# Kernel tuning notes

Hardware: AMD Instinct MI355X
Metric: run time of the kernel (lower is better)

Reference implementation:

```python
import jax, jax.numpy as jnp
import numpy as np

B, T, SEQ = 8, 129, 128
H, N, NL, NE, V = 512, 64, 4, 128, 18

def _gelu(x):
    return jax.nn.gelu(x, approximate=False)

def _conv2d(x, w, b, stride):
    y = jax.lax.conv_general_dilated(x, w, (stride, stride), 'VALID',
                                     dimension_numbers=('NCHW', 'OIHW', 'NCHW'))
    return y + b[None, :, None, None]

def _layernorm(x, g, b, eps=1e-5):
    mu = jnp.mean(x, axis=-1, keepdims=True)
    var = jnp.mean(jnp.square(x - mu), axis=-1, keepdims=True)
    return (x - mu) * jax.lax.rsqrt(var + eps) * g + b

def _s4_kernel(log_dt, A_re, A_im, C_re, C_im, L):
    # Diagonal SSM (ZOH discretization, B=1): K[h,l] = 2*Re(sum_n Ceff * exp(dt*A)^l)
    dt = jnp.exp(log_dt)[:, None]                  # [H,1]
    A = A_re + 1j * A_im                            # [H,N] complex64
    dtA = (dt * A).astype(jnp.complex64)
    C = (C_re + 1j * C_im).astype(jnp.complex64)
    Ceff = C * (jnp.exp(dtA) - 1.0) / A             # [H,N]
    vand = jnp.exp(dtA[:, :, None] * jnp.arange(L, dtype=jnp.float32))  # [H,N,L]
    return 2.0 * jnp.einsum('hn,hnl->hl', Ceff, vand).real

def _fft_conv(u, K, D):
    # u: [B,H,L]  K: [H,L]  causal conv via zero-padded FFT
    L = u.shape[-1]
    n = 2 * L
    Uf = jnp.fft.rfft(u, n=n)
    Kf = jnp.fft.rfft(K, n=n)
    y = jnp.fft.irfft(Uf * Kf[None], n=n)[..., :L]
    return y + D[None, :, None] * u

def setup_inputs() -> dict:
    key = jax.random.key(0)
    ks = jax.random.split(key, 32)
    d = {}
    d['states'] = jax.random.uniform(ks[0], (B, T, 4, 84, 84), dtype=jnp.float32)
    d['actions'] = jax.random.randint(ks[1], (B, T), 0, V)
    d['rtgs'] = jax.random.uniform(ks[2], (B, T, 1), dtype=jnp.float32)
    s = 0.02
    d['enc_w1'] = jax.random.normal(ks[3], (32, 4, 8, 8)) * s
    d['enc_b1'] = jnp.zeros((32,))
    d['enc_w2'] = jax.random.normal(ks[4], (64, 32, 4, 4)) * s
    d['enc_b2'] = jnp.zeros((64,))
    d['enc_w3'] = jax.random.normal(ks[5], (64, 64, 3, 3)) * s
    d['enc_b3'] = jnp.zeros((64,))
    d['enc_lw'] = jax.random.normal(ks[6], (3136, NE)) * s
    d['enc_lb'] = jnp.zeros((NE,))
    d['ret_w'] = jax.random.normal(ks[7], (1, NE)) * s
    d['ret_b'] = jnp.zeros((NE,))
    d['act_emb'] = jax.random.normal(ks[8], (V, NE)) * s
    d['proj_w'] = jax.random.normal(ks[9], (3 * NE, H)) * s
    d['proj_b'] = jnp.zeros((H,))
    d['pre_w'] = jax.random.normal(ks[10], (H, H)) * s
    d['pre_b'] = jnp.zeros((H,))
    d['ln_g'] = jnp.ones((NL, H))
    d['ln_b'] = jnp.zeros((NL, H))
    lo, hi = np.log(1e-3), np.log(1e-1)
    d['log_dt'] = lo + jax.random.uniform(ks[11], (NL, H)) * (hi - lo)
    d['A_re'] = -0.5 * jnp.ones((NL, H, N))
    d['A_im'] = jnp.broadcast_to(np.pi * jnp.arange(N, dtype=jnp.float32), (NL, H, N)).copy()
    d['C_re'] = jax.random.normal(ks[12], (NL, H, N)) * (0.5 ** 0.5)
    d['C_im'] = jax.random.normal(ks[13], (NL, H, N)) * (0.5 ** 0.5)
    d['Dp'] = jax.random.normal(ks[14], (NL, H))
    d['aft_w'] = jax.random.normal(ks[15], (NL, H, H)) * s
    d['aft_b'] = jnp.zeros((NL, H))
    d['out_w'] = jax.random.normal(ks[16], (H, V)) * s
    return d

def reference(states, actions, rtgs, enc_w1, enc_b1, enc_w2, enc_b2, enc_w3, enc_b3,
              enc_lw, enc_lb, ret_w, ret_b, act_emb, proj_w, proj_b, pre_w, pre_b,
              ln_g, ln_b, log_dt, A_re, A_im, C_re, C_im, Dp, aft_w, aft_b, out_w):
    S = actions.shape[1] - 1  # del_r = 1
    # state encoder over B*S frames
    x = states[:, 1:].reshape(-1, 4, 84, 84)
    x = jax.nn.relu(_conv2d(x, enc_w1, enc_b1, 4))
    x = jax.nn.relu(_conv2d(x, enc_w2, enc_b2, 2))
    x = jax.nn.relu(_conv2d(x, enc_w3, enc_b3, 1))
    se = jnp.tanh(x.reshape(x.shape[0], -1) @ enc_lw + enc_lb)          # [B*S, NE]
    ae = jnp.tanh(act_emb[actions[:, :S].reshape(-1)])                   # [B*S, NE]
    re = jnp.tanh(rtgs[:, :S].reshape(-1, 1) @ ret_w + ret_b)            # [B*S, NE]
    u = jnp.concatenate([se, ae, re], axis=-1) @ proj_w + proj_b
    u = u.reshape(states.shape[0], S, H)
    y = _gelu(u) @ pre_w + pre_b                                          # beforeblock
    for i in range(NL):
        r = _layernorm(y, ln_g[i], ln_b[i])
        v = jnp.transpose(r, (0, 2, 1))                                   # [B,H,S]
        K = _s4_kernel(log_dt[i], A_re[i], A_im[i], C_re[i], C_im[i], S)
        c = _fft_conv(v, K, Dp[i])
        c = jnp.transpose(c, (0, 2, 1))                                   # [B,S,H]
        c = _gelu(_gelu(c) @ aft_w[i] + aft_b[i])
        y = c + y                                                          # s4_resnet
    logits = y @ out_w                                                     # [B,S,V]
    return logits
```

## Files before the change

kernel.cpp:

```cpp
#include <hip/hip_runtime.h>

#define Bq 8
#define Tq 129
#define Sq 128
#define Hq 512
#define Nq 64
#define NLq 4
#define NEq 128
#define Vq 18

typedef unsigned short u16;
typedef unsigned int u32;
typedef __attribute__((ext_vector_type(8))) short short8v;
typedef __attribute__((ext_vector_type(4))) float f32x4;

__device__ __forceinline__ float gelu_f(float x) {
  return 0.5f * x * (1.0f + erff(x * 0.70710678118654752f));
}

__device__ __forceinline__ u16 f2b(float x) {
  union { float f; unsigned int u; } v; v.f = x;
  unsigned int r = v.u + 0x7FFFu + ((v.u >> 16) & 1u);
  return (u16)(r >> 16);
}

__device__ __forceinline__ float b2f_lo(u32 u) {
  union { unsigned int u; float f; } v; v.u = u << 16; return v.f;
}
__device__ __forceinline__ float b2f_hi(u32 u) {
  union { unsigned int u; float f; } v; v.u = u & 0xffff0000u; return v.f;
}

__global__ __launch_bounds__(256) void prep_k(
    const float* __restrict__ enc_lw, const float* __restrict__ proj_w,
    const float* __restrict__ pre_w, const float* __restrict__ aft_w,
    const float* __restrict__ out_w,
    const float* __restrict__ w1, const float* __restrict__ w2,
    const float* __restrict__ w3,
    u16* __restrict__ Wt_enc, u16* __restrict__ Wt_proj, u16* __restrict__ Wt_pre,
    u16* __restrict__ Wt_aft, u16* __restrict__ Wt_out,
    u16* __restrict__ B1t, u16* __restrict__ B2t, u16* __restrict__ B3t) {
  __shared__ u16 T[64][65];
  int bid = blockIdx.x;
  if (bid >= 474) {
    int i = (bid - 474) * 256 + threadIdx.x;
    if (i < 8192) {
      int n = i >> 8, k = i & 255;
      int ic = k >> 6, ky = (k >> 3) & 7, kx = k & 7;
      B1t[i] = f2b(w1[((n * 4 + ic) * 8 + ky) * 8 + kx]);
    } else if (i < 8192 + 32768) {
      int j = i - 8192;
      int n = j >> 9, k = j & 511;
      int kyx = k >> 5, ic = k & 31, ky = kyx >> 2, kx = kyx & 3;
      B2t[j] = f2b(w2[((n * 32 + ic) * 4 + ky) * 4 + kx]);
    } else if (i < 8192 + 32768 + 36864) {
      int j = i - 40960;
      int n = j / 576, k = j - n * 576;
      int ic = k & 63, kyx = k >> 6, ky = kyx / 3, kx = kyx % 3;
      B3t[j] = f2b(w3[((n * 64 + ic) * 3 + ky) * 3 + kx]);
    }
    return;
  }
  const float* src; u16* dst; int K, N, kt, nt, t;
  if (bid < 98)       { t = bid;       src = enc_lw; dst = Wt_enc;  K = 3136; N = 128; kt = t >> 1; nt = t & 1; }
  else if (bid < 146) { t = bid - 98;  src = proj_w; dst = Wt_proj; K = 384;  N = 512; kt = t >> 3; nt = t & 7; }
  else if (bid < 210) { t = bid - 146; src = pre_w;  dst = Wt_pre;  K = 512;  N = 512; kt = t >> 3; nt = t & 7; }
  else if (bid < 466) { t = bid - 210; int L = t >> 6; t &= 63;
                        src = aft_w + (size_t)L * 262144; dst = Wt_aft + (size_t)L * 262144;
                        K = 512; N = 512; kt = t >> 3; nt = t & 7; }
  else                { t = bid - 466; src = out_w;  dst = Wt_out;  K = 512;  N = 18;  kt = t;      nt = 0; }
  int k0 = kt * 64, n0 = nt * 64;
  #pragma unroll
  for (int it = 0; it < 16; it++) {
    int idx = it * 256 + threadIdx.x;
    int rr = idx >> 6, cc = idx & 63;
    float v = (n0 + cc < N) ? src[(size_t)(k0 + rr) * N + n0 + cc] : 0.f;
    T[cc][rr] = f2b(v);
  }
  __syncthreads();
  #pragma unroll
  for (int it = 0; it < 16; it++) {
    int idx = it * 256 + threadIdx.x;
    int rr = idx >> 6, cc = idx & 63;
    dst[(size_t)(n0 + rr) * K + k0 + cc] = T[rr][cc];
  }
}

__global__ __launch_bounds__(512) void conv1_mfma(const float* __restrict__ states,
    const u16* __restrict__ B1t, const float* __restrict__ bias, u16* __restrict__ out) {
  __shared__ u16 lds[28224];
  int fr = blockIdx.x;
  int b = fr >> 7, s = fr & 127;
  const float* in = states + (size_t)(b * Tq + s + 1) * 28224;
  int tid = threadIdx.x;
  #pragma unroll
  for (int it = 0; it < 14; it++) {
    int idx = tid + it * 512;
    if (idx < 7056) {
      float4 v = ((const float4*)in)[idx];
      ushort4 uv;
      uv.x = f2b(v.x); uv.y = f2b(v.y); uv.z = f2b(v.z); uv.w = f2b(v.w);
      *(ushort4*)&lds[idx * 4] = uv;
    }
  }
  int lane = tid & 63, w = tid >> 6;
  int q = lane >> 4, r = lane & 15;
  short8v bfr[2][8];
  #pragma unroll
  for (int nt = 0; nt < 2; nt++)
    #pragma unroll
    for (int ks = 0; ks < 8; ks++)
      bfr[nt][ks] = *(const short8v*)(B1t + (nt * 16 + r) * 256 + ks * 32 + q * 8);
  __syncthreads();
  for (int mt = w; mt < 25; mt += 8) {
    int m = mt * 16 + r;
    int oy = m / 20, ox = m % 20;
    f32x4 acc0 = {0.f, 0.f, 0.f, 0.f}, acc1 = {0.f, 0.f, 0.f, 0.f};
    #pragma unroll
    for (int ks = 0; ks < 8; ks++) {
      int k0 = ks * 32 + q * 8;
      int ic = k0 >> 6, ky = (k0 >> 3) & 7;
      int ai = ic * 7056 + (oy * 4 + ky) * 84 + ox * 4;
      ushort4 lo = *(const ushort4*)&lds[ai];
      ushort4 hi = *(const ushort4*)&lds[ai + 4];
      short8v av;
      av[0] = (short)lo.x; av[1] = (short)lo.y; av[2] = (short)lo.z; av[3] = (short)lo.w;
      av[4] = (short)hi.x; av[5] = (short)hi.y; av[6] = (short)hi.z; av[7] = (short)hi.w;
      acc0 = __builtin_amdgcn_mfma_f32_16x16x32_bf16(av, bfr[0][ks], acc0, 0, 0, 0);
      acc1 = __builtin_amdgcn_mfma_f32_16x16x32_bf16(av, bfr[1][ks], acc1, 0, 0, 0);
    }
    #pragma unroll
    for (int reg = 0; reg < 4; reg++) {
      int pos = mt * 16 + q * 4 + reg;
      out[(size_t)fr * 12800 + pos * 32 + r]      = f2b(fmaxf(acc0[reg] + bias[r], 0.f));
      out[(size_t)fr * 12800 + pos * 32 + 16 + r] = f2b(fmaxf(acc1[reg] + bias[16 + r], 0.f));
    }
  }
}

__global__ __launch_bounds__(256) void conv2_mfma(const u16* __restrict__ in_,
    const u16* __restrict__ B2t, const float* __restrict__ bias, u16* __restrict__ out) {
  __shared__ u16 lds[12800];
  int fr = blockIdx.x;
  int tid = threadIdx.x;
  const short8v* src = (const short8v*)(in_ + (size_t)fr * 12800);
  short8v* dst = (short8v*)lds;
  #pragma unroll
  for (int it = 0; it < 7; it++) {
    int idx = tid + it * 256;
    if (idx < 1600) dst[idx] = src[idx];
  }
  int lane = tid & 63, w = tid >> 6;
  int q = lane >> 4, r = lane & 15;
  int n = w * 16 + r;
  short8v bfr[16];
  #pragma unroll
  for (int ks = 0; ks < 16; ks++)
    bfr[ks] = *(const short8v*)(B2t + n * 512 + ks * 32 + q * 8);
  __syncthreads();
  float bn = bias[n];
  #pragma unroll
  for (int mt = 0; mt < 6; mt++) {
    int m = mt * 16 + r; if (m > 80) m = 80;
    int oy = m / 9, ox = m % 9;
    f32x4 acc = {0.f, 0.f, 0.f, 0.f};
    #pragma unroll
    for (int ks = 0; ks < 16; ks++) {
      int ky = ks >> 2, kx = ks & 3;
      int ai = ((oy * 2 + ky) * 20 + ox * 2 + kx) * 32 + q * 8;
      short8v av = *(const short8v*)&lds[ai];
      acc = __builtin_amdgcn_mfma_f32_16x16x32_bf16(av, bfr[ks], acc, 0, 0, 0);
    }
    #pragma unroll
    for (int reg = 0; reg < 4; reg++) {
      int pos = mt * 16 + q * 4 + reg;
      if (pos < 81)
        out[(size_t)fr * 5184 + pos * 64 + n] = f2b(fmaxf(acc[reg] + bn, 0.f));
    }
  }
}

__global__ __launch_bounds__(256) void conv3_mfma(const u16* __restrict__ in_,
    const u16* __restrict__ B3t, const float* __restrict__ bias, u16* __restrict__ out) {
  __shared__ u16 lds[5184];
  int fr = blockIdx.x;
  int tid = threadIdx.x;
  const short8v* src = (const short8v*)(in_ + (size_t)fr * 5184);
  short8v* dst = (short8v*)lds;
  #pragma unroll
  for (int it = 0; it < 3; it++) {
    int idx = tid + it * 256;
    if (idx < 648) dst[idx] = src[idx];
  }
  int lane = tid & 63, w = tid >> 6;
  int q = lane >> 4, r = lane & 15;
  int n = w * 16 + r;
  short8v bfr[18];
  #pragma unroll
  for (int ks = 0; ks < 18; ks++)
    bfr[ks] = *(const short8v*)(B3t + n * 576 + ks * 32 + q * 8);
  __syncthreads();
  float bn = bias[n];
  #pragma unroll
  for (int mt = 0; mt < 4; mt++) {
    int m = mt * 16 + r; if (m > 48) m = 48;
    int oy = m / 7, ox = m % 7;
    f32x4 acc = {0.f, 0.f, 0.f, 0.f};
    #pragma unroll
    for (int ks = 0; ks < 18; ks++) {
      int kyx = ks >> 1;
      int ky = kyx / 3, kx = kyx % 3;
      int ic0 = (ks & 1) * 32 + q * 8;
      int ai = ((oy + ky) * 9 + ox + kx) * 64 + ic0;
      short8v av = *(const short8v*)&lds[ai];
      acc = __builtin_amdgcn_mfma_f32_16x16x32_bf16(av, bfr[ks], acc, 0, 0, 0);
    }
    #pragma unroll
    for (int reg = 0; reg < 4; reg++) {
      int pos = mt * 16 + q * 4 + reg;
      if (pos < 49)
        out[(size_t)fr * 3136 + n * 49 + pos] = f2b(fmaxf(acc[reg] + bn, 0.f));
    }
  }
}

template<bool AF32, int EPI, bool STATS>
__global__ __launch_bounds__(256) void mgemm(const void* __restrict__ Av,
    const u16* __restrict__ Wt, const float* __restrict__ bias,
    const float* __restrict__ res, void* __restrict__ Cv,
    float2* __restrict__ part, int M, int K, int N, int ldc) {
  __shared__ u16 As[4][64][40];
  __shared__ u16 Bs[4][64][40];
  int tid = threadIdx.x;
  int bn = blockIdx.x * 64, bm = blockIdx.y * 64;
  int lane = tid & 63, w = tid >> 6;
  int q = lane >> 4, r = lane & 15;
  int wm = (w >> 1) * 32, wn = (w & 1) * 32;
  int am = tid >> 2, ak0 = (tid & 3) * 8;
  f32x4 acc[2][2] = {};
  for (int k0 = 0; k0 < K; k0 += 128) {
    #pragma unroll
    for (int st = 0; st < 4; st++) {
      int kk = k0 + st * 32 + ak0;
      if constexpr (AF32) {
        const float* A = (const float*)Av;
        const float* src = A + (size_t)(bm + am) * K + kk;
        float4 v0 = *(const float4*)src;
        float4 v1 = *(const float4*)(src + 4);
        ushort4 lo, hi;
        lo.x = f2b(v0.x); lo.y = f2b(v0.y); lo.z = f2b(v0.z); lo.w = f2b(v0.w);
        hi.x = f2b(v1.x); hi.y = f2b(v1.y); hi.z = f2b(v1.z); hi.w = f2b(v1.w);
        *(ushort4*)&As[st][am][ak0] = lo;
        *(ushort4*)&As[st][am][ak0 + 4] = hi;
      } else {
        *(short8v*)&As[st][am][ak0] =
            *(const short8v*)((const u16*)Av + (size_t)(bm + am) * K + kk);
      }
      *(short8v*)&Bs[st][am][ak0] = *(const short8v*)(Wt + (size_t)(bn + am) * K + kk);
    }
    __syncthreads();
    #pragma unroll
    for (int st = 0; st < 4; st++) {
      short8v a0 = *(const short8v*)&As[st][wm + r][q * 8];
      short8v a1 = *(const short8v*)&As[st][wm + 16 + r][q * 8];
      short8v b0 = *(const short8v*)&Bs[st][wn + r][q * 8];
      short8v b1 = *(const short8v*)&Bs[st][wn + 16 + r][q * 8];
      acc[0][0] = __builtin_amdgcn_mfma_f32_16x16x32_bf16(a0, b0, acc[0][0], 0, 0, 0);
      acc[0][1] = __builtin_amdgcn_mfma_f32_16x16x32_bf16(a0, b1, acc[0][1], 0, 0, 0);
      acc[1][0] = __builtin_amdgcn_mfma_f32_16x16x32_bf16(a1, b0, acc[1][0], 0, 0, 0);
      acc[1][1] = __builtin_amdgcn_mfma_f32_16x16x32_bf16(a1, b1, acc[1][1], 0, 0, 0);
    }
    __syncthreads();
  }
  float yv[2][2][4];
  #pragma unroll
  for (int ms = 0; ms < 2; ms++) {
    #pragma unroll
    for (int ns = 0; ns < 2; ns++) {
      #pragma unroll
      for (int reg = 0; reg < 4; reg++) {
        int m = bm + wm + ms * 16 + q * 4 + reg;
        int n = bn + wn + ns * 16 + r;
        if (n < N) {
          float v = acc[ms][ns][reg] + (bias ? bias[n] : 0.f);
          if (EPI == 0) { ((float*)Cv)[(size_t)m * ldc + n] = v; yv[ms][ns][reg] = v; }
          if (EPI == 2) ((u16*)Cv)[(size_t)m * ldc + n] = f2b(gelu_f(v));
          if (EPI == 3) {
            float o = gelu_f(v) + res[(size_t)m * ldc + n];
            ((float*)Cv)[(size_t)m * ldc + n] = o; yv[ms][ns][reg] = o;
          }
        }
      }
    }
  }
  if constexpr (STATS) {
    #pragma unroll
    for (int ms = 0; ms < 2; ms++) {
      #pragma unroll
      for (int reg = 0; reg < 4; reg++) {
        float s = yv[ms][0][reg] + yv[ms][1][reg];
        float s2 = yv[ms][0][reg] * yv[ms][0][reg] + yv[ms][1][reg] * yv[ms][1][reg];
        #pragma unroll
        for (int o = 1; o <= 8; o <<= 1) {
          s += __shfl_xor(s, o);
          s2 += __shfl_xor(s2, o);
        }
        if (r == 0) {
          int m = bm + wm + ms * 16 + q * 4 + reg;
          part[(size_t)(blockIdx.x * 2 + (w & 1)) * 1024 + m] = make_float2(s, s2);
        }
      }
    }
  }
}

__global__ __launch_bounds__(256) void enc_gemm(const u16* __restrict__ A,
    const u16* __restrict__ Wt, float* __restrict__ Cp) {
  __shared__ u16 As[64][40];
  __shared__ u16 Bs[64][40];
  int tid = threadIdx.x;
  int bn = blockIdx.x * 64, bm = blockIdx.y * 64, kc = blockIdx.z;
  int lane = tid & 63, w = tid >> 6;
  int q = lane >> 4, r = lane & 15;
  int wm = (w >> 1) * 32, wn = (w & 1) * 32;
  int am = tid >> 2, ak = (tid & 3) * 8;
  f32x4 acc[2][2] = {};
  int kend = kc * 448 + 448;
  for (int k0 = kc * 448; k0 < kend; k0 += 32) {
    *(short8v*)&As[am][ak] = *(const short8v*)(A + (size_t)(bm + am) * 3136 + k0 + ak);
    *(short8v*)&Bs[am][ak] = *(const short8v*)(Wt + (size_t)(bn + am) * 3136 + k0 + ak);
    __syncthreads();
    short8v a0 = *(const short8v*)&As[wm + r][q * 8];
    short8v a1 = *(const short8v*)&As[wm + 16 + r][q * 8];
    short8v b0 = *(const short8v*)&Bs[wn + r][q * 8];
    short8v b1 = *(const short8v*)&Bs[wn + 16 + r][q * 8];
    acc[0][0] = __builtin_amdgcn_mfma_f32_16x16x32_bf16(a0, b0, acc[0][0], 0, 0, 0);
    acc[0][1] = __builtin_amdgcn_mfma_f32_16x16x32_bf16(a0, b1, acc[0][1], 0, 0, 0);
    acc[1][0] = __builtin_amdgcn_mfma_f32_16x16x32_bf16(a1, b0, acc[1][0], 0, 0, 0);
    acc[1][1] = __builtin_amdgcn_mfma_f32_16x16x32_bf16(a1, b1, acc[1][1], 0, 0, 0);
    __syncthreads();
  }
  #pragma unroll
  for (int ms = 0; ms < 2; ms++)
    #pragma unroll
    for (int ns = 0; ns < 2; ns++)
      #pragma unroll
      for (int reg = 0; reg < 4; reg++) {
        int m = bm + wm + ms * 16 + q * 4 + reg;
        int n = bn + wn + ns * 16 + r;
        Cp[(size_t)(kc * 1024 + m) * 128 + n] = acc[ms][ns][reg];
      }
}

__global__ __launch_bounds__(256) void embedred_k(const float* __restrict__ Cp,
    const float* __restrict__ enc_lb, const int* __restrict__ actions,
    const float* __restrict__ rtgs, const float* __restrict__ act_emb,
    const float* __restrict__ ret_w, const float* __restrict__ ret_b,
    u16* __restrict__ uin) {
  int f = blockIdx.x;
  int b = f >> 7, s = f & 127;
  int e = threadIdx.x;
  if (e < 128) {
    float sum = enc_lb[e];
    #pragma unroll
    for (int kc = 0; kc < 7; kc++) sum += Cp[(size_t)(kc * 1024 + f) * 128 + e];
    uin[(size_t)f * 384 + e] = f2b(tanhf(sum));
    uin[(size_t)f * 384 + 256 + e] =
        f2b(tanhf(fmaf(rtgs[b * Tq + s], ret_w[e], ret_b[e])));
  } else {
    int ee = e - 128;
    int a = actions[b * Tq + s];
    uin[(size_t)f * 384 + 128 + ee] = f2b(tanhf(act_emb[a * NEq + ee]));
  }
}

__global__ __launch_bounds__(64) void s4k_gen(const float* __restrict__ log_dt,
    const float* __restrict__ A_re, const float* __restrict__ A_im,
    const float* __restrict__ C_re, const float* __restrict__ C_im,
    u16* __restrict__ Ktb) {
  __shared__ float con[64][129];
  int lh = blockIdx.x;
  int n = threadIdx.x;
  float dt = expf(log_dt[lh]);
  float ar = A_re[(size_t)lh * Nq + n], ai = A_im[(size_t)lh * Nq + n];
  float al = dt * ar, be = dt * ai;
  float er = expf(al);
  float wr = er * cosf(be), wi = er * sinf(be);
  float zr = wr - 1.0f, zi = wi;
  float den = 1.0f / (ar * ar + ai * ai);
  float tr = (zr * ar + zi * ai) * den, ti = (zi * ar - zr * ai) * den;
  float Cr = C_re[(size_t)lh * Nq + n], Ci = C_im[(size_t)lh * Nq + n];
  float cr = Cr * tr - Ci * ti, ci = Cr * ti + Ci * tr;
  float curr = 1.0f, curi = 0.0f;
  for (int l = 0; l < Sq; l++) {
    con[n][l] = cr * curr - ci * curi;
    float nr = curr * wr - curi * wi;
    curi = curr * wi + curi * wr;
    curr = nr;
  }
  __syncthreads();
  int layer = lh >> 9, h = lh & 511;
  #pragma unroll
  for (int li = n; li < Sq; li += 64) {
    float s = 0.f;
    for (int j = 0; j < 64; j++) s += con[j][li];
    Ktb[((size_t)layer * Sq + li) * Hq + h] = f2b(2.0f * s);
  }
}

__global__ __launch_bounds__(256) void sconv_fused(const float* __restrict__ y,
    const float2* __restrict__ part, const float* __restrict__ g,
    const float* __restrict__ bta, const u16* __restrict__ Kt,
    const float* __restrict__ D, u16* __restrict__ cact) {
  __shared__ u32 P[16][140];
  __shared__ u32 KL[16][132];
  __shared__ float2 statl[128];
  int hc = blockIdx.x, b = blockIdx.y;
  int t = threadIdx.x;
  int h0 = hc * 32;
  if (t < 128) {
    float s = 0.f, s2 = 0.f;
    #pragma unroll
    for (int pc = 0; pc < 16; pc++) {
      float2 pp = part[(size_t)pc * 1024 + b * Sq + t];
      s += pp.x; s2 += pp.y;
    }
    float mu = s * (1.f / Hq);
    float var = s2 * (1.f / Hq) - mu * mu;
    statl[t] = make_float2(mu, rsqrtf(var + 1e-5f));
  }
  if (t < 16) {
    #pragma unroll
    for (int i = 0; i < 8; i++) P[t][i] = 0;
  }
  #pragma unroll
  for (int it = 0; it < 8; it++) {
    int idx = it * 256 + t;
    int p = idx & 15, j = idx >> 4;
    KL[p][j] = *(const u32*)(Kt + (size_t)j * Hq + h0 + 2 * p);
  }
  __syncthreads();
  #pragma unroll
  for (int it = 0; it < 8; it++) {
    int idx = it * 256 + t;
    int p = idx & 15, s = idx >> 4;
    int row = b * Sq + s;
    float2 v = *(const float2*)(y + (size_t)row * Hq + h0 + 2 * p);
    float2 st = statl[s];
    float2 gg = *(const float2*)(g + h0 + 2 * p);
    float2 bb = *(const float2*)(bta + h0 + 2 * p);
    float r0 = (v.x - st.x) * st.y * gg.x + bb.x;
    float r1 = (v.y - st.x) * st.y * gg.y + bb.y;
    P[p][8 + s] = (u32)f2b(r0) | ((u32)f2b(r1) << 16);
  }
  __syncthreads();
  int p = t & 15, sg = t >> 4;
  int s0 = sg * 8;
  float acc0[8], acc1[8];
  float2 d2 = *(const float2*)(D + h0 + 2 * p);
  #pragma unroll
  for (int k = 0; k < 8; k++) {
    u32 rv = P[p][8 + s0 + k];
    acc0[k] = d2.x * b2f_lo(rv);
    acc1[k] = d2.y * b2f_hi(rv);
  }
  for (int jb = 0; jb <= sg; jb++) {
    int base = (sg - jb) * 8;
    u32 wv[16], kv[8];
    *(uint4*)&wv[0]  = *(const uint4*)&P[p][base];
    *(uint4*)&wv[4]  = *(const uint4*)&P[p][base + 4];
    *(uint4*)&wv[8]  = *(const uint4*)&P[p][base + 8];
    *(uint4*)&wv[12] = *(const uint4*)&P[p][base + 12];
    *(uint4*)&kv[0]  = *(const uint4*)&KL[p][jb * 8];
    *(uint4*)&kv[4]  = *(const uint4*)&KL[p][jb * 8 + 4];
    float wlo[16], whi[16], klo[8], khi[8];
    #pragma unroll
    for (int i = 0; i < 16; i++) { wlo[i] = b2f_lo(wv[i]); whi[i] = b2f_hi(wv[i]); }
    #pragma unroll
    for (int i = 0; i < 8; i++) { klo[i] = b2f_lo(kv[i]); khi[i] = b2f_hi(kv[i]); }
    #pragma unroll
    for (int jo = 0; jo < 8; jo++)
      #pragma unroll
      for (int k = 0; k < 8; k++) {
        acc0[k] = fmaf(klo[jo], wlo[8 + k - jo], acc0[k]);
        acc1[k] = fmaf(khi[jo], whi[8 + k - jo], acc1[k]);
      }
  }
  #pragma unroll
  for (int k = 0; k < 8; k++) {
    int s = s0 + k;
    u32 outv = (u32)f2b(gelu_f(acc0[k])) | ((u32)f2b(gelu_f(acc1[k])) << 16);
    *(u32*)(cact + ((size_t)(b * Sq + s)) * Hq + h0 + 2 * p) = outv;
  }
}

extern "C" void kernel_launch(void* const* d_in, const int* in_sizes, int n_in,
                              void* d_out, int out_size, void* d_ws, size_t ws_size,
                              hipStream_t stream) {
  const float* states  = (const float*)d_in[0];
  const int*   actions = (const int*)  d_in[1];
  const float* rtgs    = (const float*)d_in[2];
  const float* enc_w1  = (const float*)d_in[3];
  const float* enc_b1  = (const float*)d_in[4];
  const float* enc_w2  = (const float*)d_in[5];
  const float* enc_b2  = (const float*)d_in[6];
  const float* enc_w3  = (const float*)d_in[7];
  const float* enc_b3  = (const float*)d_in[8];
  const float* enc_lw  = (const float*)d_in[9];
  const float* enc_lb  = (const float*)d_in[10];
  const float* ret_w   = (const float*)d_in[11];
  const float* ret_b   = (const float*)d_in[12];
  const float* act_emb = (const float*)d_in[13];
  const float* proj_w  = (const float*)d_in[14];
  const float* proj_b  = (const float*)d_in[15];
  const float* pre_w   = (const float*)d_in[16];
  const float* pre_b   = (const float*)d_in[17];
  const float* ln_g    = (const float*)d_in[18];
  const float* ln_b    = (const float*)d_in[19];
  const float* log_dt  = (const float*)d_in[20];
  const float* A_re    = (const float*)d_in[21];
  const float* A_im    = (const float*)d_in[22];
  const float* C_re    = (const float*)d_in[23];
  const float* C_im    = (const float*)d_in[24];
  const float* Dp      = (const float*)d_in[25];
  const float* aft_w   = (const float*)d_in[26];
  const float* aft_b   = (const float*)d_in[27];
  const float* out_w   = (const float*)d_in[28];

  u16* Wt_enc  = (u16*)d_ws;
  u16* Wt_proj = Wt_enc + 401408;
  u16* Wt_pre  = Wt_proj + 196608;
  u16* Wt_aft  = Wt_pre + 262144;
  u16* Wt_out  = Wt_aft + 1048576;
  u16* B1t = Wt_out + 32768;
  u16* B2t = B1t + 8192;
  u16* B3t = B2t + 32768;
  u16* o1  = B3t + 36864;
  u16* o2  = o1 + 13107200;
  u16* x3b = o2 + 5308416;
  u16* uin = x3b + 3211264;
  u16* uact = uin + 393216;
  u16* cact = uact + 524288;
  u16* Ktb  = cact + 524288;
  float* y    = (float*)(Ktb + 262144);
  float* Cp   = y + 524288;
  float2* part = (float2*)(Cp + 917504);

  prep_k<<<778, 256, 0, stream>>>(enc_lw, proj_w, pre_w, aft_w, out_w,
                                  enc_w1, enc_w2, enc_w3,
                                  Wt_enc, Wt_proj, Wt_pre, Wt_aft, Wt_out,
                                  B1t, B2t, B3t);
  conv1_mfma<<<1024, 512, 0, stream>>>(states, B1t, enc_b1, o1);
  conv2_mfma<<<1024, 256, 0, stream>>>(o1, B2t, enc_b2, o2);
  conv3_mfma<<<1024, 256, 0, stream>>>(o2, B3t, enc_b3, x3b);
  enc_gemm<<<dim3(2, 16, 7), 256, 0, stream>>>(x3b, Wt_enc, Cp);
  embedred_k<<<1024, 256, 0, stream>>>(Cp, enc_lb, actions, rtgs, act_emb,
                                       ret_w, ret_b, uin);
  mgemm<false, 2, false><<<dim3(8, 16), 256, 0, stream>>>(uin, Wt_proj, proj_b,
      nullptr, uact, nullptr, 1024, 384, 512, 512);
  mgemm<false, 0, true><<<dim3(8, 16), 256, 0, stream>>>(uact, Wt_pre, pre_b,
      nullptr, y, part, 1024, 512, 512, 512);
  s4k_gen<<<2048, 64, 0, stream>>>(log_dt, A_re, A_im, C_re, C_im, Ktb);

  for (int i = 0; i < NLq; i++) {
    sconv_fused<<<dim3(16, 8), 256, 0, stream>>>(y, part, ln_g + i * Hq,
                                                 ln_b + i * Hq,
                                                 Ktb + (size_t)i * Sq * Hq,
                                                 Dp + i * Hq, cact);
    mgemm<false, 3, true><<<dim3(8, 16), 256, 0, stream>>>(cact,
        Wt_aft + (size_t)i * Hq * Hq, aft_b + i * Hq, y, y, part,
        1024, 512, 512, 512);
  }
  mgemm<true, 0, false><<<dim3(1, 16), 256, 0, stream>>>(y, Wt_out, nullptr,
      nullptr, (float*)d_out, nullptr, 1024, 512, Vq, Vq);
}
```

Measured before the change: 225.2 us.

## Fuse tail stages into one persistent kernel with grid-wide barriers

Replaces the embedding, projection, pre-block GEMM, four sconv+GEMM layer pairs and the output GEMM with a single persistent kernel of 128 blocks. The stages are separated by atomic-counter grid barriers, and the barrier counters are zeroed in prep_k. The aim is to remove about a dozen kernel launches and the gaps between them in the small-latency tail. In exchange it relies on all 128 blocks being resident at once, adds spin-wait barrier cost, and shares one LDS buffer across the stages.

Measured after the change: 446.6 us. 1.98x slower.

```diff
diff --git a/kernel.cpp b/kernel.cpp
--- a/kernel.cpp
+++ b/kernel.cpp
@@ -8,6 +8,7 @@
 #define NLq 4
 #define NEq 128
 #define Vq 18
+#define NBLK 128
 
 typedef unsigned short u16;
 typedef unsigned int u32;
@@ -29,6 +30,17 @@
 }
 __device__ __forceinline__ float b2f_hi(u32 u) {
   union { unsigned int u; float f; } v; v.u = u & 0xffff0000u; return v.f;
+}
+
+__device__ __forceinline__ void gsync(int* bar, int id) {
+  __threadfence();
+  __syncthreads();
+  if (threadIdx.x == 0) {
+    atomicAdd(&bar[id], 1);
+    while (atomicAdd(&bar[id], 0) < NBLK) __builtin_amdgcn_s_sleep(2);
+  }
+  __syncthreads();
+  __threadfence();
 }
 
 __global__ __launch_bounds__(256) void prep_k(
@@ -39,10 +51,12 @@
     const float* __restrict__ w3,
     u16* __restrict__ Wt_enc, u16* __restrict__ Wt_proj, u16* __restrict__ Wt_pre,
     u16* __restrict__ Wt_aft, u16* __restrict__ Wt_out,
-    u16* __restrict__ B1t, u16* __restrict__ B2t, u16* __restrict__ B3t) {
+    u16* __restrict__ B1t, u16* __restrict__ B2t, u16* __restrict__ B3t,
+    int* __restrict__ bar) {
   __shared__ u16 T[64][65];
   int bid = blockIdx.x;
   if (bid >= 474) {
+    if (bid == 474 && threadIdx.x < 32) bar[threadIdx.x] = 0;
     int i = (bid - 474) * 256 + threadIdx.x;
     if (i < 8192) {
       int n = i >> 8, k = i & 255;
@@ -220,96 +234,6 @@
       int pos = mt * 16 + q * 4 + reg;
       if (pos < 49)
         out[(size_t)fr * 3136 + n * 49 + pos] = f2b(fmaxf(acc[reg] + bn, 0.f));
-    }
-  }
-}
-
-template<bool AF32, int EPI, bool STATS>
-__global__ __launch_bounds__(256) void mgemm(const void* __restrict__ Av,
-    const u16* __restrict__ Wt, const float* __restrict__ bias,
-    const float* __restrict__ res, void* __restrict__ Cv,
-    float2* __restrict__ part, int M, int K, int N, int ldc) {
-  __shared__ u16 As[4][64][40];
-  __shared__ u16 Bs[4][64][40];
-  int tid = threadIdx.x;
-  int bn = blockIdx.x * 64, bm = blockIdx.y * 64;
-  int lane = tid & 63, w = tid >> 6;
-  int q = lane >> 4, r = lane & 15;
-  int wm = (w >> 1) * 32, wn = (w & 1) * 32;
-  int am = tid >> 2, ak0 = (tid & 3) * 8;
-  f32x4 acc[2][2] = {};
-  for (int k0 = 0; k0 < K; k0 += 128) {
-    #pragma unroll
-    for (int st = 0; st < 4; st++) {
-      int kk = k0 + st * 32 + ak0;
-      if constexpr (AF32) {
-        const float* A = (const float*)Av;
-        const float* src = A + (size_t)(bm + am) * K + kk;
-        float4 v0 = *(const float4*)src;
-        float4 v1 = *(const float4*)(src + 4);
-        ushort4 lo, hi;
-        lo.x = f2b(v0.x); lo.y = f2b(v0.y); lo.z = f2b(v0.z); lo.w = f2b(v0.w);
-        hi.x = f2b(v1.x); hi.y = f2b(v1.y); hi.z = f2b(v1.z); hi.w = f2b(v1.w);
-        *(ushort4*)&As[st][am][ak0] = lo;
-        *(ushort4*)&As[st][am][ak0 + 4] = hi;
-      } else {
-        *(short8v*)&As[st][am][ak0] =
-            *(const short8v*)((const u16*)Av + (size_t)(bm + am) * K + kk);
-      }
-      *(short8v*)&Bs[st][am][ak0] = *(const short8v*)(Wt + (size_t)(bn + am) * K + kk);
-    }
-    __syncthreads();
-    #pragma unroll
-    for (int st = 0; st < 4; st++) {
-      short8v a0 = *(const short8v*)&As[st][wm + r][q * 8];
-      short8v a1 = *(const short8v*)&As[st][wm + 16 + r][q * 8];
-      short8v b0 = *(const short8v*)&Bs[st][wn + r][q * 8];
-      short8v b1 = *(const short8v*)&Bs[st][wn + 16 + r][q * 8];
-      acc[0][0] = __builtin_amdgcn_mfma_f32_16x16x32_bf16(a0, b0, acc[0][0], 0, 0, 0);
-      acc[0][1] = __builtin_amdgcn_mfma_f32_16x16x32_bf16(a0, b1, acc[0][1], 0, 0, 0);
-      acc[1][0] = __builtin_amdgcn_mfma_f32_16x16x32_bf16(a1, b0, acc[1][0], 0, 0, 0);
-      acc[1][1] = __builtin_amdgcn_mfma_f32_16x16x32_bf16(a1, b1, acc[1][1], 0, 0, 0);
-    }
-    __syncthreads();
-  }
-  float yv[2][2][4];
-  #pragma unroll
-  for (int ms = 0; ms < 2; ms++) {
-    #pragma unroll
-    for (int ns = 0; ns < 2; ns++) {
-      #pragma unroll
-      for (int reg = 0; reg < 4; reg++) {
-        int m = bm + wm + ms * 16 + q * 4 + reg;
-        int n = bn + wn + ns * 16 + r;
-        if (n < N) {
-          float v = acc[ms][ns][reg] + (bias ? bias[n] : 0.f);
-          if (EPI == 0) { ((float*)Cv)[(size_t)m * ldc + n] = v; yv[ms][ns][reg] = v; }
-          if (EPI == 2) ((u16*)Cv)[(size_t)m * ldc + n] = f2b(gelu_f(v));
-          if (EPI == 3) {
-            float o = gelu_f(v) + res[(size_t)m * ldc + n];
-            ((float*)Cv)[(size_t)m * ldc + n] = o; yv[ms][ns][reg] = o;
-          }
-        }
-      }
-    }
-  }
-  if constexpr (STATS) {
-    #pragma unroll
-    for (int ms = 0; ms < 2; ms++) {
-      #pragma unroll
-      for (int reg = 0; reg < 4; reg++) {
-        float s = yv[ms][0][reg] + yv[ms][1][reg];
-        float s2 = yv[ms][0][reg] * yv[ms][0][reg] + yv[ms][1][reg] * yv[ms][1][reg];
-        #pragma unroll
-        for (int o = 1; o <= 8; o <<= 1) {
-          s += __shfl_xor(s, o);
-          s2 += __shfl_xor(s2, o);
-        }
-        if (r == 0) {
-          int m = bm + wm + ms * 16 + q * 4 + reg;
-          part[(size_t)(blockIdx.x * 2 + (w & 1)) * 1024 + m] = make_float2(s, s2);
-        }
-      }
     }
   }
 }
@@ -352,28 +276,6 @@
       }
 }
 
-__global__ __launch_bounds__(256) void embedred_k(const float* __restrict__ Cp,
-    const float* __restrict__ enc_lb, const int* __restrict__ actions,
-    const float* __restrict__ rtgs, const float* __restrict__ act_emb,
-    const float* __restrict__ ret_w, const float* __restrict__ ret_b,
-    u16* __restrict__ uin) {
-  int f = blockIdx.x;
-  int b = f >> 7, s = f & 127;
-  int e = threadIdx.x;
-  if (e < 128) {
-    float sum = enc_lb[e];
-    #pragma unroll
-    for (int kc = 0; kc < 7; kc++) sum += Cp[(size_t)(kc * 1024 + f) * 128 + e];
-    uin[(size_t)f * 384 + e] = f2b(tanhf(sum));
-    uin[(size_t)f * 384 + 256 + e] =
-        f2b(tanhf(fmaf(rtgs[b * Tq + s], ret_w[e], ret_b[e])));
-  } else {
-    int ee = e - 128;
-    int a = actions[b * Tq + s];
-    uin[(size_t)f * 384 + 128 + ee] = f2b(tanhf(act_emb[a * NEq + ee]));
-  }
-}
-
 __global__ __launch_bounds__(64) void s4k_gen(const float* __restrict__ log_dt,
     const float* __restrict__ A_re, const float* __restrict__ A_im,
     const float* __restrict__ C_re, const float* __restrict__ C_im,
@@ -408,14 +310,111 @@
   }
 }
 
-__global__ __launch_bounds__(256) void sconv_fused(const float* __restrict__ y,
-    const float2* __restrict__ part, const float* __restrict__ g,
-    const float* __restrict__ bta, const u16* __restrict__ Kt,
-    const float* __restrict__ D, u16* __restrict__ cact) {
-  __shared__ u32 P[16][140];
-  __shared__ u32 KL[16][132];
-  __shared__ float2 statl[128];
-  int hc = blockIdx.x, b = blockIdx.y;
+struct TailP {
+  const float* Cp; const float* enc_lb; const int* actions;
+  const float* rtgs; const float* act_emb; const float* ret_w; const float* ret_b;
+  u16* uin; u16* uact; u16* cact;
+  const u16* Wt_proj; const u16* Wt_pre; const u16* Wt_aft; const u16* Wt_out;
+  const float* proj_b; const float* pre_b; const float* aft_b;
+  const float* ln_g; const float* ln_b; const float* Dp;
+  const u16* Ktb; float* y; float2* part; float* outp; int* bar;
+};
+
+template<bool AF32, int EPI, bool STATS>
+__device__ void gemm_dev(int bx, int by, const void* Av, const u16* Wt,
+    const float* bias, const float* res, void* Cv, float2* part,
+    int K, int N, int ldc, u16* sm) {
+  u16 (*As)[64][40] = reinterpret_cast<u16(*)[64][40]>(sm);
+  u16 (*Bs)[64][40] = reinterpret_cast<u16(*)[64][40]>(sm + 10240);
+  int tid = threadIdx.x;
+  int bn = bx * 64, bm = by * 64;
+  int lane = tid & 63, w = tid >> 6;
+  int q = lane >> 4, r = lane & 15;
+  int wm = (w >> 1) * 32, wn = (w & 1) * 32;
+  int am = tid >> 2, ak0 = (tid & 3) * 8;
+  f32x4 acc[2][2] = {};
+  for (int k0 = 0; k0 < K; k0 += 128) {
+    #pragma unroll
+    for (int st = 0; st < 4; st++) {
+      int kk = k0 + st * 32 + ak0;
+      if constexpr (AF32) {
+        const float* A = (const float*)Av;
+        const float* src = A + (size_t)(bm + am) * K + kk;
+        float4 v0 = *(const float4*)src;
+        float4 v1 = *(const float4*)(src + 4);
+        ushort4 lo, hi;
+        lo.x = f2b(v0.x); lo.y = f2b(v0.y); lo.z = f2b(v0.z); lo.w = f2b(v0.w);
+        hi.x = f2b(v1.x); hi.y = f2b(v1.y); hi.z = f2b(v1.z); hi.w = f2b(v1.w);
+        *(ushort4*)&As[st][am][ak0] = lo;
+        *(ushort4*)&As[st][am][ak0 + 4] = hi;
+      } else {
+        *(short8v*)&As[st][am][ak0] =
+            *(const short8v*)((const u16*)Av + (size_t)(bm + am) * K + kk);
+      }
+      *(short8v*)&Bs[st][am][ak0] = *(const short8v*)(Wt + (size_t)(bn + am) * K + kk);
+    }
+    __syncthreads();
+    #pragma unroll
+    for (int st = 0; st < 4; st++) {
+      short8v a0 = *(const short8v*)&As[st][wm + r][q * 8];
+      short8v a1 = *(const short8v*)&As[st][wm + 16 + r][q * 8];
+      short8v b0 = *(const short8v*)&Bs[st][wn + r][q * 8];
+      short8v b1 = *(const short8v*)&Bs[st][wn + 16 + r][q * 8];
+      acc[0][0] = __builtin_amdgcn_mfma_f32_16x16x32_bf16(a0, b0, acc[0][0], 0, 0, 0);
+      acc[0][1] = __builtin_amdgcn_mfma_f32_16x16x32_bf16(a0, b1, acc[0][1], 0, 0, 0);
+      acc[1][0] = __builtin_amdgcn_mfma_f32_16x16x32_bf16(a1, b0, acc[1][0], 0, 0, 0);
+      acc[1][1] = __builtin_amdgcn_mfma_f32_16x16x32_bf16(a1, b1, acc[1][1], 0, 0, 0);
+    }
+    __syncthreads();
+  }
+  float yv[2][2][4];
+  #pragma unroll
+  for (int ms = 0; ms < 2; ms++) {
+    #pragma unroll
+    for (int ns = 0; ns < 2; ns++) {
+      #pragma unroll
+      for (int reg = 0; reg < 4; reg++) {
+        int m = bm + wm + ms * 16 + q * 4 + reg;
+        int n = bn + wn + ns * 16 + r;
+        if (n < N) {
+          float v = acc[ms][ns][reg] + (bias ? bias[n] : 0.f);
+          if (EPI == 0) { ((float*)Cv)[(size_t)m * ldc + n] = v; yv[ms][ns][reg] = v; }
+          if (EPI == 2) ((u16*)Cv)[(size_t)m * ldc + n] = f2b(gelu_f(v));
+          if (EPI == 3) {
+            float o = gelu_f(v) + res[(size_t)m * ldc + n];
+            ((float*)Cv)[(size_t)m * ldc + n] = o; yv[ms][ns][reg] = o;
+          }
+        }
+      }
+    }
+  }
+  if constexpr (STATS) {
+    #pragma unroll
+    for (int ms = 0; ms < 2; ms++) {
+      #pragma unroll
+      for (int reg = 0; reg < 4; reg++) {
+        float s = yv[ms][0][reg] + yv[ms][1][reg];
+        float s2 = yv[ms][0][reg] * yv[ms][0][reg] + yv[ms][1][reg] * yv[ms][1][reg];
+        #pragma unroll
+        for (int o = 1; o <= 8; o <<= 1) {
+          s += __shfl_xor(s, o);
+          s2 += __shfl_xor(s2, o);
+        }
+        if (r == 0) {
+          int m = bm + wm + ms * 16 + q * 4 + reg;
+          part[(size_t)(bx * 2 + (w & 1)) * 1024 + m] = make_float2(s, s2);
+        }
+      }
+    }
+  }
+}
+
+__device__ void sconv_dev(int hc, int b, const float* y, const float2* part,
+    const float* g, const float* bta, const u16* Kt, const float* D,
+    u16* cact, u16* sm) {
+  u32 (*P)[140] = reinterpret_cast<u32(*)[140]>(sm);
+  u32 (*KL)[132] = reinterpret_cast<u32(*)[132]>((char*)sm + 8960);
+  float2* statl = reinterpret_cast<float2*>((char*)sm + 8960 + 8448);
   int t = threadIdx.x;
   int h0 = hc * 32;
   if (t < 128) {
@@ -492,6 +491,50 @@
     u32 outv = (u32)f2b(gelu_f(acc0[k])) | ((u32)f2b(gelu_f(acc1[k])) << 16);
     *(u32*)(cact + ((size_t)(b * Sq + s)) * Hq + h0 + 2 * p) = outv;
   }
+}
+
+__device__ void embed_dev(int f, const TailP& P) {
+  int b = f >> 7, s = f & 127;
+  int e = threadIdx.x;
+  if (e < 128) {
+    float sum = P.enc_lb[e];
+    #pragma unroll
+    for (int kc = 0; kc < 7; kc++) sum += P.Cp[(size_t)(kc * 1024 + f) * 128 + e];
+    P.uin[(size_t)f * 384 + e] = f2b(tanhf(sum));
+    P.uin[(size_t)f * 384 + 256 + e] =
+        f2b(tanhf(fmaf(P.rtgs[b * Tq + s], P.ret_w[e], P.ret_b[e])));
+  } else {
+    int ee = e - 128;
+    int a = P.actions[b * Tq + s];
+    P.uin[(size_t)f * 384 + 128 + ee] = f2b(tanhf(P.act_emb[a * NEq + ee]));
+  }
+}
+
+__global__ __launch_bounds__(256) void tail_k(TailP P) {
+  __shared__ __align__(16) u16 smem[20480];
+  int blk = blockIdx.x;
+  int id = 0;
+  #pragma unroll
+  for (int i = 0; i < 8; i++) embed_dev(blk * 8 + i, P);
+  gsync(P.bar, id++);
+  gemm_dev<false, 2, false>(blk & 7, blk >> 3, P.uin, P.Wt_proj, P.proj_b,
+                            nullptr, P.uact, nullptr, 384, 512, 512, smem);
+  gsync(P.bar, id++);
+  gemm_dev<false, 0, true>(blk & 7, blk >> 3, P.uact, P.Wt_pre, P.pre_b,
+                           nullptr, P.y, P.part, 512, 512, 512, smem);
+  gsync(P.bar, id++);
+  for (int L = 0; L < NLq; L++) {
+    sconv_dev(blk & 15, blk >> 4, P.y, P.part, P.ln_g + L * Hq, P.ln_b + L * Hq,
+              P.Ktb + (size_t)L * Sq * Hq, P.Dp + L * Hq, P.cact, smem);
+    gsync(P.bar, id++);
+    gemm_dev<false, 3, true>(blk & 7, blk >> 3, P.cact,
+                             P.Wt_aft + (size_t)L * Hq * Hq, P.aft_b + L * Hq,
+                             P.y, P.y, P.part, 512, 512, 512, smem);
+    gsync(P.bar, id++);
+  }
+  if (blk < 16)
+    gemm_dev<true, 0, false>(0, blk, P.y, P.Wt_out, nullptr, nullptr,
+                             P.outp, nullptr, 512, Vq, Vq, smem);
 }
 
 extern "C" void kernel_launch(void* const* d_in, const int* in_sizes, int n_in,
@@ -545,32 +588,25 @@
   float* y    = (float*)(Ktb + 262144);
   float* Cp   = y + 524288;
   float2* part = (float2*)(Cp + 917504);
+  int* bar    = (int*)(part + 16384);
 
   prep_k<<<778, 256, 0, stream>>>(enc_lw, proj_w, pre_w, aft_w, out_w,
                                   enc_w1, enc_w2, enc_w3,
                                   Wt_enc, Wt_proj, Wt_pre, Wt_aft, Wt_out,
-                                  B1t, B2t, B3t);
+                                  B1t, B2t, B3t, bar);
   conv1_mfma<<<1024, 512, 0, stream>>>(states, B1t, enc_b1, o1);
   conv2_mfma<<<1024, 256, 0, stream>>>(o1, B2t, enc_b2, o2);
   conv3_mfma<<<1024, 256, 0, stream>>>(o2, B3t, enc_b3, x3b);
   enc_gemm<<<dim3(2, 16, 7), 256, 0, stream>>>(x3b, Wt_enc, Cp);
-  embedred_k<<<1024, 256, 0, stream>>>(Cp, enc_lb, actions, rtgs, act_emb,
-                                       ret_w, ret_b, uin);
-  mgemm<false, 2, false><<<dim3(8, 16), 256, 0, stream>>>(uin, Wt_proj, proj_b,
-      nullptr, uact, nullptr, 1024, 384, 512, 512);
-  mgemm<false, 0, true><<<dim3(8, 16), 256, 0, stream>>>(uact, Wt_pre, pre_b,
-      nullptr, y, part, 1024, 512, 512, 512);
   s4k_gen<<<2048, 64, 0, stream>>>(log_dt, A_re, A_im, C_re, C_im, Ktb);
 
-  for (int i = 0; i < NLq; i++) {
-    sconv_fused<<<dim3(16, 8), 256, 0, stream>>>(y, part, ln_g + i * Hq,
-                                                 ln_b + i * Hq,
-                                                 Ktb + (size_t)i * Sq * Hq,
-                                                 Dp + i * Hq, cact);
-    mgemm<false, 3, true><<<dim3(8, 16), 256, 0, stream>>>(cact,
-        Wt_aft + (size_t)i * Hq * Hq, aft_b + i * Hq, y, y, part,
-        1024, 512, 512, 512);
-  }
-  mgemm<true, 0, false><<<dim3(1, 16), 256, 0, stream>>>(y, Wt_out, nullptr,
-      nullptr, (float*)d_out, nullptr, 1024, 512, Vq, Vq);
-}
+  TailP tp;
+  tp.Cp = Cp; tp.enc_lb = enc_lb; tp.actions = actions;
+  tp.rtgs = rtgs; tp.act_emb = act_emb; tp.ret_w = ret_w; tp.ret_b = ret_b;
+  tp.uin = uin; tp.uact = uact; tp.cact = cact;
+  tp.Wt_proj = Wt_proj; tp.Wt_pre = Wt_pre; tp.Wt_aft = Wt_aft; tp.Wt_out = Wt_out;
+  tp.proj_b = proj_b; tp.pre_b = pre_b; tp.aft_b = aft_b;
+  tp.ln_g = ln_g; tp.ln_b = ln_b; tp.Dp = Dp;
+  tp.Ktb = Ktb; tp.y = y; tp.part = part; tp.outp = (float*)d_out; tp.bar = bar;
+  tail_k<<<NBLK, 256, 0, stream>>>(tp);
+}
```

## Fuse conv2 and conv3 into one kernel and batch conv1 input loads

Applied to the files above, without the earlier changes.

Merges the conv2 and conv3 kernels so that conv2's output stays in shared memory and conv3 reads it from there, removing the global write and reread of the intermediate activation and one kernel launch. conv1 now issues all of its float4 global loads into registers before converting to bf16 and storing to LDS, which puts more memory requests in flight at once. The fused kernel uses more LDS per block, and the staging array raises register pressure in conv1, both of which may lower occupancy.

Measured after the change: 217.2 us. -3.6%, faster.

```diff
diff --git a/kernel.cpp b/kernel.cpp
--- a/kernel.cpp
+++ b/kernel.cpp
@@ -93,13 +93,19 @@
   int b = fr >> 7, s = fr & 127;
   const float* in = states + (size_t)(b * Tq + s + 1) * 28224;
   int tid = threadIdx.x;
+  float4 stg[14];
+  #pragma unroll
+  for (int it = 0; it < 14; it++) {
+    int idx = tid + it * 512;
+    if (idx < 7056) stg[it] = ((const float4*)in)[idx];
+  }
   #pragma unroll
   for (int it = 0; it < 14; it++) {
     int idx = tid + it * 512;
     if (idx < 7056) {
-      float4 v = ((const float4*)in)[idx];
       ushort4 uv;
-      uv.x = f2b(v.x); uv.y = f2b(v.y); uv.z = f2b(v.z); uv.w = f2b(v.w);
+      uv.x = f2b(stg[it].x); uv.y = f2b(stg[it].y);
+      uv.z = f2b(stg[it].z); uv.w = f2b(stg[it].w);
       *(ushort4*)&lds[idx * 4] = uv;
     }
   }
@@ -138,13 +144,16 @@
   }
 }
 
-__global__ __launch_bounds__(256) void conv2_mfma(const u16* __restrict__ in_,
-    const u16* __restrict__ B2t, const float* __restrict__ bias, u16* __restrict__ out) {
-  __shared__ u16 lds[12800];
+__global__ __launch_bounds__(256) void conv23_mfma(const u16* __restrict__ o1,
+    const u16* __restrict__ B2t, const u16* __restrict__ B3t,
+    const float* __restrict__ b2, const float* __restrict__ b3,
+    u16* __restrict__ x3b) {
+  __shared__ u16 o1l[12800];
+  __shared__ u16 o2l[5184];
   int fr = blockIdx.x;
   int tid = threadIdx.x;
-  const short8v* src = (const short8v*)(in_ + (size_t)fr * 12800);
-  short8v* dst = (short8v*)lds;
+  const short8v* src = (const short8v*)(o1 + (size_t)fr * 12800);
+  short8v* dst = (short8v*)o1l;
   #pragma unroll
   for (int it = 0; it < 7; it++) {
     int idx = tid + it * 256;
@@ -153,12 +162,12 @@
   int lane = tid & 63, w = tid >> 6;
   int q = lane >> 4, r = lane & 15;
   int n = w * 16 + r;
-  short8v bfr[16];
+  short8v bfr2[16];
   #pragma unroll
   for (int ks = 0; ks < 16; ks++)
-    bfr[ks] = *(const short8v*)(B2t + n * 512 + ks * 32 + q * 8);
-  __syncthreads();
-  float bn = bias[n];
+    bfr2[ks] = *(const short8v*)(B2t + n * 512 + ks * 32 + q * 8);
+  __syncthreads();
+  float bn2 = b2[n];
   #pragma unroll
   for (int mt = 0; mt < 6; mt++) {
     int m = mt * 16 + r; if (m > 80) m = 80;
@@ -168,39 +177,22 @@
     for (int ks = 0; ks < 16; ks++) {
       int ky = ks >> 2, kx = ks & 3;
       int ai = ((oy * 2 + ky) * 20 + ox * 2 + kx) * 32 + q * 8;
-      short8v av = *(const short8v*)&lds[ai];
-      acc = __builtin_amdgcn_mfma_f32_16x16x32_bf16(av, bfr[ks], acc, 0, 0, 0);
+      short8v av = *(const short8v*)&o1l[ai];
+      acc = __builtin_amdgcn_mfma_f32_16x16x32_bf16(av, bfr2[ks], acc, 0, 0, 0);
     }
     #pragma unroll
     for (int reg = 0; reg < 4; reg++) {
       int pos = mt * 16 + q * 4 + reg;
       if (pos < 81)
-        out[(size_t)fr * 5184 + pos * 64 + n] = f2b(fmaxf(acc[reg] + bn, 0.f));
-    }
-  }
-}
-
-__global__ __launch_bounds__(256) void conv3_mfma(const u16* __restrict__ in_,
-    const u16* __restrict__ B3t, const float* __restrict__ bias, u16* __restrict__ out) {
-  __shared__ u16 lds[5184];
-  int fr = blockIdx.x;
-  int tid = threadIdx.x;
-  const short8v* src = (const short8v*)(in_ + (size_t)fr * 5184);
-  short8v* dst = (short8v*)lds;
-  #pragma unroll
-  for (int it = 0; it < 3; it++) {
-    int idx = tid + it * 256;
-    if (idx < 648) dst[idx] = src[idx];
-  }
-  int lane = tid & 63, w = tid >> 6;
-  int q = lane >> 4, r = lane & 15;
-  int n = w * 16 + r;
-  short8v bfr[18];
+        o2l[pos * 64 + n] = f2b(fmaxf(acc[reg] + bn2, 0.f));
+    }
+  }
+  short8v bfr3[18];
   #pragma unroll
   for (int ks = 0; ks < 18; ks++)
-    bfr[ks] = *(const short8v*)(B3t + n * 576 + ks * 32 + q * 8);
-  __syncthreads();
-  float bn = bias[n];
+    bfr3[ks] = *(const short8v*)(B3t + n * 576 + ks * 32 + q * 8);
+  __syncthreads();
+  float bn3 = b3[n];
   #pragma unroll
   for (int mt = 0; mt < 4; mt++) {
     int m = mt * 16 + r; if (m > 48) m = 48;
@@ -212,14 +204,14 @@
       int ky = kyx / 3, kx = kyx % 3;
       int ic0 = (ks & 1) * 32 + q * 8;
       int ai = ((oy + ky) * 9 + ox + kx) * 64 + ic0;
-      short8v av = *(const short8v*)&lds[ai];
-      acc = __builtin_amdgcn_mfma_f32_16x16x32_bf16(av, bfr[ks], acc, 0, 0, 0);
+      short8v av = *(const short8v*)&o2l[ai];
+      acc = __builtin_amdgcn_mfma_f32_16x16x32_bf16(av, bfr3[ks], acc, 0, 0, 0);
     }
     #pragma unroll
     for (int reg = 0; reg < 4; reg++) {
       int pos = mt * 16 + q * 4 + reg;
       if (pos < 49)
-        out[(size_t)fr * 3136 + n * 49 + pos] = f2b(fmaxf(acc[reg] + bn, 0.f));
+        x3b[(size_t)fr * 3136 + n * 49 + pos] = f2b(fmaxf(acc[reg] + bn3, 0.f));
     }
   }
 }
@@ -536,8 +528,7 @@
   u16* B2t = B1t + 8192;
   u16* B3t = B2t + 32768;
   u16* o1  = B3t + 36864;
-  u16* o2  = o1 + 13107200;
-  u16* x3b = o2 + 5308416;
+  u16* x3b = o1 + 13107200;
   u16* uin = x3b + 3211264;
   u16* uact = uin + 393216;
   u16* cact = uact + 524288;
@@ -551,8 +542,7 @@
                                   Wt_enc, Wt_proj, Wt_pre, Wt_aft, Wt_out,
                                   B1t, B2t, B3t);
   conv1_mfma<<<1024, 512, 0, stream>>>(states, B1t, enc_b1, o1);
-  conv2_mfma<<<1024, 256, 0, stream>>>(o1, B2t, enc_b2, o2);
-  conv3_mfma<<<1024, 256, 0, stream>>>(o2, B3t, enc_b3, x3b);
+  conv23_mfma<<<1024, 256, 0, stream>>>(o1, B2t, B3t, enc_b2, enc_b3, x3b);
   enc_gemm<<<dim3(2, 16, 7), 256, 0, stream>>>(x3b, Wt_enc, Cp);
   embedred_k<<<1024, 256, 0, stream>>>(Cp, enc_lb, actions, rtgs, act_emb,
                                        ret_w, ret_b, uin);
```
